# Kernel tuning notes

Measured on AMD Instinct MI355X. Metric: run time of the kernel, lower is better.

## Reference

```python
import jax, jax.numpy as jnp
import numpy as np

WS = 7          # window size
SHIFT = 3       # shift size
HEADS = 4
DIM = 128
PRETRAIN = 7    # pretrain_window_size
LN_EPS = 1e-3   # keras LayerNormalization default epsilon

# ---- constant relative-position structures (match TF meshgrid 'xy' indexing) ----
def _rel_index(ws):
    coords = np.stack(np.meshgrid(np.arange(ws), np.arange(ws)))  # [2, ws, ws] (xy)
    flat = coords.reshape(2, -1)
    rel = (flat[:, :, None] - flat[:, None, :]).transpose(1, 2, 0)  # [N, N, 2]
    ry = (rel[..., 0] + ws - 1) * (2 * ws - 1)
    rx = rel[..., 1] + ws - 1
    return (ry + rx).reshape(-1)  # [N*N]

def _rel_table(ws, pretrain):
    h = np.arange(-(ws - 1), ws, dtype=np.float32)
    t = np.stack(np.meshgrid(h, h), axis=-1)[None]  # [1, 2ws-1, 2ws-1, 2] (xy)
    t = t / (pretrain - 1)
    t = t * (8.0 / (pretrain - 1))
    return np.sign(t) * np.log1p(np.abs(t)) / np.log(8.0)

REL_INDEX = jnp.asarray(_rel_index(WS))
REL_TABLE = jnp.asarray(_rel_table(WS, PRETRAIN))


def layernorm(x, g, b, eps=LN_EPS):
    m = jnp.mean(x, axis=-1, keepdims=True)
    v = jnp.mean(jnp.square(x - m), axis=-1, keepdims=True)
    return (x - m) / jnp.sqrt(v + eps) * g + b


def setup_inputs() -> dict:
    key = jax.random.key(0)
    ks = jax.random.split(key, 16)
    B, H, W, C = 64, 56, 56, DIM
    nW = (H // WS) * (W // WS)
    hid = int(C * 4.0)
    rpe_h = 512
    def w(k, shape, scale=0.02):
        return jax.random.normal(k, shape, dtype=jnp.float32) * scale
    return {
        "x": jax.random.normal(ks[0], (B, H, W, C), dtype=jnp.float32),
        "mask_matrix": jax.random.normal(ks[1], (nW, WS * WS, WS * WS), dtype=jnp.float32),
        "norm1_g": jnp.ones((C,), jnp.float32),
        "norm1_b": jnp.zeros((C,), jnp.float32),
        "qkv_w": w(ks[2], (C, 3 * C)),
        "q_bias": jnp.zeros((C,), jnp.float32),
        "v_bias": jnp.zeros((C,), jnp.float32),
        "logit_scale": jnp.full((HEADS, 1, 1), np.log(10.0), jnp.float32),
        "rpe_w1": w(ks[3], (2, rpe_h)),
        "rpe_b1": jnp.zeros((rpe_h,), jnp.float32),
        "rpe_w2": w(ks[4], (rpe_h, HEADS)),
        "proj_w": w(ks[5], (C, C)),
        "proj_b": jnp.zeros((C,), jnp.float32),
        "norm2_g": jnp.ones((C,), jnp.float32),
        "norm2_b": jnp.zeros((C,), jnp.float32),
        "fc1_w": w(ks[6], (C, hid)),
        "fc1_b": jnp.zeros((hid,), jnp.float32),
        "fc2_w": w(ks[7], (hid, C)),
        "fc2_b": jnp.zeros((C,), jnp.float32),
    }


def reference(x, mask_matrix, norm1_g, norm1_b, qkv_w, q_bias, v_bias, logit_scale,
              rpe_w1, rpe_b1, rpe_w2, proj_w, proj_b, norm2_g, norm2_b,
              fc1_w, fc1_b, fc2_w, fc2_b):
    B, H, W, C = x.shape
    N = WS * WS
    hd = C // HEADS
    shortcut = x

    # cyclic shift + window partition -> [Bw, N, C]
    xs = jnp.roll(x, (-SHIFT, -SHIFT), axis=(1, 2))
    xw = xs.reshape(B, H // WS, WS, W // WS, WS, C).transpose(0, 1, 3, 2, 4, 5)
    xw = xw.reshape(-1, N, C)
    Bw = xw.shape[0]

    # qkv with (q_bias, 0, v_bias)
    qkv_bias = jnp.concatenate([q_bias, jnp.zeros_like(v_bias), v_bias])
    qkv = (xw @ qkv_w + qkv_bias).reshape(Bw, N, 3, HEADS, hd).transpose(2, 0, 3, 1, 4)
    q, k, v = qkv[0], qkv[1], qkv[2]  # [Bw, HEADS, N, hd]

    # cosine attention with clamped learnable log-scale
    scale = jnp.exp(jnp.minimum(logit_scale, jnp.log(1.0 / 0.01)))
    qn = q / jnp.sqrt(jnp.maximum(jnp.sum(q * q, -1, keepdims=True), 1e-12))
    kn = k / jnp.sqrt(jnp.maximum(jnp.sum(k * k, -1, keepdims=True), 1e-12))
    attn = jnp.einsum('bhnd,bhmd->bhnm', qn, kn) * scale

    # continuous relative position bias via tiny MLP
    t = REL_TABLE.reshape(-1, 2)                          # [(2ws-1)^2, 2]
    bias_table = jax.nn.relu(t @ rpe_w1 + rpe_b1) @ rpe_w2  # [(2ws-1)^2, HEADS]
    pb = bias_table[REL_INDEX].reshape(N, N, HEADS).transpose(2, 0, 1)
    attn = attn + (16.0 * jax.nn.sigmoid(pb))[None]

    # shift mask
    nW = mask_matrix.shape[0]
    attn = attn.reshape(Bw // nW, nW, HEADS, N, N) + mask_matrix[None, :, None]
    attn = attn.reshape(-1, HEADS, N, N)

    attn = jax.nn.softmax(attn, axis=-1)
    out = jnp.einsum('bhnm,bhmd->bhnd', attn, v).transpose(0, 2, 1, 3).reshape(Bw, N, C)
    out = out @ proj_w + proj_b

    # window reverse + un-shift
    out = out.reshape(B, H // WS, W // WS, WS, WS, C).transpose(0, 1, 3, 2, 4, 5)
    out = out.reshape(B, H, W, C)
    out = jnp.roll(out, (SHIFT, SHIFT), axis=(1, 2))

    # post-norm residuals (SwinV2 style)
    x = shortcut + layernorm(out, norm1_g, norm1_b)
    h = jax.nn.gelu(x @ fc1_w + fc1_b, approximate=False) @ fc2_w + fc2_b
    x = x + layernorm(h, norm2_g, norm2_b)
    return x
```

## Files before the change

kernel.cpp:

```cpp
#include <hip/hip_runtime.h>

typedef __attribute__((ext_vector_type(8))) short bf16x8;
typedef __attribute__((ext_vector_type(4))) float f32x4;

__device__ __forceinline__ short f2bf(float f) {
    union { float f; unsigned u; } c; c.f = f;
    unsigned r = c.u + 0x7FFFu + ((c.u >> 16) & 1u);
    return (short)(r >> 16);
}
__device__ __forceinline__ float bf2f(short s) {
    union { unsigned u; float f; } c; c.u = ((unsigned)(unsigned short)s) << 16;
    return c.f;
}

#define MFMA(a, b, c) __builtin_amdgcn_mfma_f32_16x16x32_bf16((a), (b), (c), 0, 0, 0)

#define WS_QKVWT   0
#define WS_PROJWT  98304
#define WS_FC1WT   131072
#define WS_FC2WT   262144
#define WS_PB16    393216
#define WS_COMB    434176

__global__ __launch_bounds__(256) void k_prep_w(
    const float* __restrict__ qkv_w, const float* __restrict__ proj_w,
    const float* __restrict__ fc1_w, const float* __restrict__ fc2_w,
    short* __restrict__ qkv_wt, short* __restrict__ proj_wt,
    short* __restrict__ fc1_wt, short* __restrict__ fc2_wt) {
    int id = blockIdx.x * 256 + threadIdx.x;
    if (id < 49152) {
        int n = id >> 7, k = id & 127;
        qkv_wt[id] = f2bf(qkv_w[k * 384 + n]);
    } else if (id < 65536) {
        int i = id - 49152; int n = i >> 7, k = i & 127;
        proj_wt[i] = f2bf(proj_w[k * 128 + n]);
    } else if (id < 131072) {
        int i = id - 65536; int n = i >> 7, k = i & 127;
        fc1_wt[i] = f2bf(fc1_w[k * 512 + n]);
    } else if (id < 196608) {
        int i = id - 131072; int n = i >> 9, k = i & 511;
        fc2_wt[i] = f2bf(fc2_w[k * 128 + n]);
    }
}

__device__ __forceinline__ float rpe_f(float u) {
    float us = u * (2.0f / 9.0f);
    return copysignf(log1pf(fabsf(us)), us) * 0.48089834696298783f;
}

__global__ __launch_bounds__(256) void k_prep_bias(
    const float* __restrict__ w1, const float* __restrict__ b1,
    const float* __restrict__ w2, float* __restrict__ pb16) {
    __shared__ float bt[169][4];
    int tid = threadIdx.x;
    if (tid < 169) {
        int i = tid / 13, j = tid - 13 * (tid / 13);
        float t0 = rpe_f((float)(j - 6));
        float t1 = rpe_f((float)(i - 6));
        float a0 = 0.f, a1 = 0.f, a2 = 0.f, a3 = 0.f;
        for (int k = 0; k < 512; ++k) {
            float r = fmaxf(t0 * w1[k] + t1 * w1[512 + k] + b1[k], 0.f);
            a0 += r * w2[k * 4 + 0]; a1 += r * w2[k * 4 + 1];
            a2 += r * w2[k * 4 + 2]; a3 += r * w2[k * 4 + 3];
        }
        bt[tid][0] = a0; bt[tid][1] = a1; bt[tid][2] = a2; bt[tid][3] = a3;
    }
    __syncthreads();
    for (int idx = tid; idx < 9604; idx += 256) {
        int h = idx / 2401, pq = idx - 2401 * h;
        int p = pq / 49, q = pq - 49 * p;
        int dx = p % 7 - q % 7;
        int dy = p / 7 - q / 7;
        int m = (dx + 6) * 13 + (dy + 6);
        float v = bt[m][h];
        pb16[idx] = 16.0f / (1.0f + expf(-v));
    }
}

__global__ __launch_bounds__(256) void k_combine(
    const float* __restrict__ mask, const float* __restrict__ pb16,
    float* __restrict__ comb) {
    int idx = blockIdx.x * 256 + threadIdx.x;
    if (idx >= 614656) return;
    int w = idx / 9604, rem = idx - 9604 * w;
    int pq = rem % 2401;
    comb[idx] = mask[w * 2401 + pq] + pb16[rem];
}

__global__ __launch_bounds__(256) void k_attn(
    const float* __restrict__ x, const float* __restrict__ comb,
    const short* __restrict__ qkv_wt, const short* __restrict__ proj_wt,
    const float* __restrict__ q_bias, const float* __restrict__ v_bias,
    const float* __restrict__ logit_scale, const float* __restrict__ proj_b,
    const float* __restrict__ n1g, const float* __restrict__ n1b,
    float* __restrict__ out) {
    __shared__ short sm[29504];
    short* q_s = sm;
    short* k_s = sm + 7840;
    short* v_s = sm + 15680;
    short* p_s = sm + 24896;
    short* xw  = sm;

    const int tid = threadIdx.x;
    const int lane = tid & 63, wv = tid >> 6;
    const int n16 = lane & 15, q4 = lane >> 4;
    const int wb = blockIdx.x;
    const int bb = wb >> 6, widx = wb & 63;
    const int wy = widx >> 3, wx = widx & 7;

    if (tid < 196) {
        int tok = tid >> 2, part = tid & 3;
        int ty = tok / 7, tx = tok - 7 * ty;
        int sy = wy * 7 + ty + 3; if (sy >= 56) sy -= 56;
        int sx = wx * 7 + tx + 3; if (sx >= 56) sx -= 56;
        const float* src = x + (((bb * 56 + sy) * 56 + sx) << 7) + part * 32;
        short* dst = xw + tok * 136 + part * 32;
#pragma unroll
        for (int j = 0; j < 8; ++j) {
            float4 v = *(const float4*)(src + j * 4);
            short4 o;
            o.x = f2bf(v.x); o.y = f2bf(v.y); o.z = f2bf(v.z); o.w = f2bf(v.w);
            *(short4*)(dst + j * 4) = o;
        }
    }
    __syncthreads();

    bf16x8 afr[4][4];
#pragma unroll
    for (int mt = 0; mt < 4; ++mt)
#pragma unroll
        for (int ks = 0; ks < 4; ++ks)
            afr[mt][ks] = *(const bf16x8*)(xw + (mt * 16 + n16) * 136 + ks * 32 + q4 * 8);

    f32x4 acc[6][4];
#pragma unroll
    for (int ntl = 0; ntl < 6; ++ntl) {
        int n = (wv * 6 + ntl) * 16 + n16;
        bf16x8 bfr[4];
#pragma unroll
        for (int ks = 0; ks < 4; ++ks)
            bfr[ks] = *(const bf16x8*)(qkv_wt + n * 128 + ks * 32 + q4 * 8);
#pragma unroll
        for (int mt = 0; mt < 4; ++mt) {
            f32x4 a = {0.f, 0.f, 0.f, 0.f};
#pragma unroll
            for (int ks = 0; ks < 4; ++ks) a = MFMA(afr[mt][ks], bfr[ks], a);
            acc[ntl][mt] = a;
        }
    }
    __syncthreads();

#pragma unroll
    for (int ntl = 0; ntl < 6; ++ntl) {
        int n = (wv * 6 + ntl) * 16 + n16;
        int sec = n >> 7, h = (n >> 5) & 3, chn = n & 31;
        float bias = (sec == 0) ? q_bias[n] : ((sec == 2) ? v_bias[n & 127] : 0.f);
#pragma unroll
        for (int mt = 0; mt < 4; ++mt) {
#pragma unroll
            for (int reg = 0; reg < 4; ++reg) {
                int r = mt * 16 + q4 * 4 + reg;
                float val = acc[ntl][mt][reg] + bias;
                if (sec == 2) {
                    v_s[h * 2304 + chn * 72 + r] = (r < 49) ? f2bf(val) : (short)0;
                } else if (r < 49) {
                    short* base = sec ? k_s : q_s;
                    base[h * 1960 + r * 40 + chn] = f2bf(val);
                }
            }
        }
    }
    __syncthreads();

    for (int i = tid; i < 392; i += 256) {
        int which = (i >= 196) ? 1 : 0;
        int rem = i - which * 196;
        int h = rem / 49, t = rem - 49 * h;
        short* row = (which ? k_s : q_s) + h * 1960 + t * 40;
        float vv[32]; float ss = 0.f;
#pragma unroll
        for (int j = 0; j < 8; ++j) {
            short4 s4 = *(const short4*)(row + j * 4);
            vv[j*4+0] = bf2f(s4.x); vv[j*4+1] = bf2f(s4.y);
            vv[j*4+2] = bf2f(s4.z); vv[j*4+3] = bf2f(s4.w);
            ss += vv[j*4+0]*vv[j*4+0] + vv[j*4+1]*vv[j*4+1]
                + vv[j*4+2]*vv[j*4+2] + vv[j*4+3]*vv[j*4+3];
        }
        float inv = 1.0f / sqrtf(fmaxf(ss, 1e-12f));
        if (!which) inv *= expf(fminf(logit_scale[h], 4.6051702f));
#pragma unroll
        for (int j = 0; j < 8; ++j) {
            short4 o;
            o.x = f2bf(vv[j*4+0]*inv); o.y = f2bf(vv[j*4+1]*inv);
            o.z = f2bf(vv[j*4+2]*inv); o.w = f2bf(vv[j*4+3]*inv);
            *(short4*)(row + j * 4) = o;
        }
    }
    __syncthreads();

    const int rb = wv * 16;
#pragma unroll 1
    for (int h = 0; h < 4; ++h) {
        bf16x8 aq = *(const bf16x8*)(q_s + h * 1960 + (rb + n16) * 40 + q4 * 8);
        f32x4 s[4];
#pragma unroll
        for (int nt = 0; nt < 4; ++nt) {
            bf16x8 bk = *(const bf16x8*)(k_s + h * 1960 + (nt * 16 + n16) * 40 + q4 * 8);
            f32x4 z = {0.f, 0.f, 0.f, 0.f};
            s[nt] = MFMA(aq, bk, z);
        }
#pragma unroll
        for (int nt = 0; nt < 4; ++nt) {
            int c = nt * 16 + n16;
#pragma unroll
            for (int reg = 0; reg < 4; ++reg) {
                int r = rb + q4 * 4 + reg;
                float val;
                if (c < 49) {
                    val = s[nt][reg];
                    if (r < 49) val += comb[((widx * 4 + h) * 49 + r) * 49 + c];
                } else val = -INFINITY;
                s[nt][reg] = val;
            }
        }
#pragma unroll
        for (int reg = 0; reg < 4; ++reg) {
            float m = fmaxf(fmaxf(s[0][reg], s[1][reg]), fmaxf(s[2][reg], s[3][reg]));
#pragma unroll
            for (int d = 1; d < 16; d <<= 1) m = fmaxf(m, __shfl_xor(m, d, 64));
            float e0 = expf(s[0][reg] - m), e1 = expf(s[1][reg] - m);
            float e2 = expf(s[2][reg] - m), e3 = expf(s[3][reg] - m);
            float sum = e0 + e1 + e2 + e3;
#pragma unroll
            for (int d = 1; d < 16; d <<= 1) sum += __shfl_xor(sum, d, 64);
            float inv = 1.0f / sum;
            s[0][reg] = e0 * inv; s[1][reg] = e1 * inv;
            s[2][reg] = e2 * inv; s[3][reg] = e3 * inv;
        }
#pragma unroll
        for (int nt = 0; nt < 4; ++nt)
#pragma unroll
            for (int reg = 0; reg < 4; ++reg)
                p_s[wv * 1152 + (q4 * 4 + reg) * 72 + nt * 16 + n16] = f2bf(s[nt][reg]);

        bf16x8 ap0 = *(const bf16x8*)(p_s + wv * 1152 + n16 * 72 + q4 * 8);
        bf16x8 ap1 = *(const bf16x8*)(p_s + wv * 1152 + n16 * 72 + 32 + q4 * 8);
#pragma unroll
        for (int nt2 = 0; nt2 < 2; ++nt2) {
            bf16x8 bv0 = *(const bf16x8*)(v_s + h * 2304 + (nt2 * 16 + n16) * 72 + q4 * 8);
            bf16x8 bv1 = *(const bf16x8*)(v_s + h * 2304 + (nt2 * 16 + n16) * 72 + 32 + q4 * 8);
            f32x4 z = {0.f, 0.f, 0.f, 0.f};
            f32x4 o = MFMA(ap0, bv0, z);
            o = MFMA(ap1, bv1, o);
#pragma unroll
            for (int reg = 0; reg < 4; ++reg) {
                int r = rb + q4 * 4 + reg;
                if (r < 49)
                    q_s[h * 1960 + r * 40 + nt2 * 16 + n16] = f2bf(o[reg]);
            }
        }
    }

    bf16x8 apj[4];
#pragma unroll
    for (int ks = 0; ks < 4; ++ks)
        apj[ks] = *(const bf16x8*)(q_s + ks * 1960 + (rb + n16) * 40 + q4 * 8);
    f32x4 pacc[8];
#pragma unroll
    for (int nt = 0; nt < 8; ++nt) {
        f32x4 a = {0.f, 0.f, 0.f, 0.f};
#pragma unroll
        for (int ks = 0; ks < 4; ++ks) {
            bf16x8 bp = *(const bf16x8*)(proj_wt + (nt * 16 + n16) * 128 + ks * 32 + q4 * 8);
            a = MFMA(apj[ks], bp, a);
        }
        pacc[nt] = a;
    }

    float pbv[8], gv[8], bvv[8];
#pragma unroll
    for (int nt = 0; nt < 8; ++nt) {
        int c = nt * 16 + n16;
        pbv[nt] = proj_b[c]; gv[nt] = n1g[c]; bvv[nt] = n1b[c];
    }
#pragma unroll
    for (int reg = 0; reg < 4; ++reg) {
        int r = rb + q4 * 4 + reg;
        float vals[8]; float s1 = 0.f, s2 = 0.f;
#pragma unroll
        for (int nt = 0; nt < 8; ++nt) {
            float v = pacc[nt][reg] + pbv[nt];
            vals[nt] = v; s1 += v; s2 += v * v;
        }
#pragma unroll
        for (int d = 1; d < 16; d <<= 1) {
            s1 += __shfl_xor(s1, d, 64);
            s2 += __shfl_xor(s2, d, 64);
        }
        float mean = s1 * 0.0078125f;
        float var = s2 * 0.0078125f - mean * mean;
        float inv = 1.0f / sqrtf(var + 1e-3f);
        if (r < 49) {
            int ty = r / 7, tx = r - 7 * ty;
            int fy = wy * 7 + ty + 3; if (fy >= 56) fy -= 56;
            int fx = wx * 7 + tx + 3; if (fx >= 56) fx -= 56;
            int gb = ((bb * 56 + fy) * 56 + fx) << 7;
#pragma unroll
            for (int nt = 0; nt < 8; ++nt) {
                int c = nt * 16 + n16;
                float ln = (vals[nt] - mean) * inv * gv[nt] + bvv[nt];
                out[gb + c] = x[gb + c] + ln;
            }
        }
    }
}

__global__ __launch_bounds__(256) void k_mlp(
    float* __restrict__ io, const short* __restrict__ fc1_wt,
    const short* __restrict__ fc2_wt, const float* __restrict__ fc1_b,
    const float* __restrict__ fc2_b, const float* __restrict__ n2g,
    const float* __restrict__ n2b) {
    __shared__ short sm2[26624];
    short* xt = sm2;
    short* hc = sm2 + 17408;

    const int tid = threadIdx.x;
    const int lane = tid & 63, wv = tid >> 6;
    const int n16 = lane & 15, q4 = lane >> 4;
    const int T0 = blockIdx.x * 128;

    {
        int trow = tid >> 1, half = tid & 1;
        const float* src = io + (T0 + trow) * 128 + half * 64;
        short* dst = xt + trow * 136 + half * 64;
#pragma unroll
        for (int j = 0; j < 16; ++j) {
            float4 v = *(const float4*)(src + j * 4);
            short4 o;
            o.x = f2bf(v.x); o.y = f2bf(v.y); o.z = f2bf(v.z); o.w = f2bf(v.w);
            *(short4*)(dst + j * 4) = o;
        }
    }
    __syncthreads();

    f32x4 oacc[2][8];
#pragma unroll
    for (int i2 = 0; i2 < 2; ++i2)
#pragma unroll
        for (int nt = 0; nt < 8; ++nt) oacc[i2][nt] = (f32x4){0.f, 0.f, 0.f, 0.f};

#pragma unroll 1
    for (int ch = 0; ch < 8; ++ch) {
        int nrow = ch * 64 + wv * 16 + n16;
        bf16x8 b1[4];
#pragma unroll
        for (int ks = 0; ks < 4; ++ks)
            b1[ks] = *(const bf16x8*)(fc1_wt + nrow * 128 + ks * 32 + q4 * 8);
        float fb = fc1_b[nrow];
#pragma unroll
        for (int mt = 0; mt < 8; ++mt) {
            f32x4 a = {0.f, 0.f, 0.f, 0.f};
#pragma unroll
            for (int ks = 0; ks < 4; ++ks) {
                bf16x8 af = *(const bf16x8*)(xt + (mt * 16 + n16) * 136 + ks * 32 + q4 * 8);
                a = MFMA(af, b1[ks], a);
            }
#pragma unroll
            for (int reg = 0; reg < 4; ++reg) {
                float v = a[reg] + fb;
                float g = 0.5f * v * (1.0f + erff(v * 0.7071067811865476f));
                hc[(mt * 16 + q4 * 4 + reg) * 72 + wv * 16 + n16] = f2bf(g);
            }
        }
        __syncthreads();
        bf16x8 a2[2][2];
#pragma unroll
        for (int i2 = 0; i2 < 2; ++i2) {
            int m = (wv + i2 * 4) * 16;
#pragma unroll
            for (int ks2 = 0; ks2 < 2; ++ks2)
                a2[i2][ks2] = *(const bf16x8*)(hc + (m + n16) * 72 + ks2 * 32 + q4 * 8);
        }
#pragma unroll
        for (int nt2 = 0; nt2 < 8; ++nt2) {
#pragma unroll
            for (int ks2 = 0; ks2 < 2; ++ks2) {
                bf16x8 b2 = *(const bf16x8*)(fc2_wt + (nt2 * 16 + n16) * 512 + ch * 64 + ks2 * 32 + q4 * 8);
                oacc[0][nt2] = MFMA(a2[0][ks2], b2, oacc[0][nt2]);
                oacc[1][nt2] = MFMA(a2[1][ks2], b2, oacc[1][nt2]);
            }
        }
        __syncthreads();
    }

    float f2bv[8], g2[8], b2v[8];
#pragma unroll
    for (int nt2 = 0; nt2 < 8; ++nt2) {
        int c = nt2 * 16 + n16;
        f2bv[nt2] = fc2_b[c]; g2[nt2] = n2g[c]; b2v[nt2] = n2b[c];
    }
#pragma unroll
    for (int i2 = 0; i2 < 2; ++i2) {
        int rb2 = (wv + i2 * 4) * 16;
#pragma unroll
        for (int reg = 0; reg < 4; ++reg) {
            int r = rb2 + q4 * 4 + reg;
            float vals[8]; float s1 = 0.f, s2 = 0.f;
#pragma unroll
            for (int nt2 = 0; nt2 < 8; ++nt2) {
                float v = oacc[i2][nt2][reg] + f2bv[nt2];
                vals[nt2] = v; s1 += v; s2 += v * v;
            }
#pragma unroll
            for (int d = 1; d < 16; d <<= 1) {
                s1 += __shfl_xor(s1, d, 64);
                s2 += __shfl_xor(s2, d, 64);
            }
            float mean = s1 * 0.0078125f;
            float var = s2 * 0.0078125f - mean * mean;
            float inv = 1.0f / sqrtf(var + 1e-3f);
            int gb = (T0 + r) * 128;
#pragma unroll
            for (int nt2 = 0; nt2 < 8; ++nt2) {
                int c = nt2 * 16 + n16;
                float ln = (vals[nt2] - mean) * inv * g2[nt2] + b2v[nt2];
                io[gb + c] = io[gb + c] + ln;
            }
        }
    }
}

extern "C" void kernel_launch(void* const* d_in, const int* in_sizes, int n_in,
                              void* d_out, int out_size, void* d_ws, size_t ws_size,
                              hipStream_t stream) {
    const float* x      = (const float*)d_in[0];
    const float* mask   = (const float*)d_in[1];
    const float* n1g    = (const float*)d_in[2];
    const float* n1b    = (const float*)d_in[3];
    const float* qkv_w  = (const float*)d_in[4];
    const float* q_bias = (const float*)d_in[5];
    const float* v_bias = (const float*)d_in[6];
    const float* lscale = (const float*)d_in[7];
    const float* rpe_w1 = (const float*)d_in[8];
    const float* rpe_b1 = (const float*)d_in[9];
    const float* rpe_w2 = (const float*)d_in[10];
    const float* proj_w = (const float*)d_in[11];
    const float* proj_b = (const float*)d_in[12];
    const float* n2g    = (const float*)d_in[13];
    const float* n2b    = (const float*)d_in[14];
    const float* fc1_w  = (const float*)d_in[15];
    const float* fc1_b  = (const float*)d_in[16];
    const float* fc2_w  = (const float*)d_in[17];
    const float* fc2_b  = (const float*)d_in[18];

    char* ws = (char*)d_ws;
    short* qkv_wt  = (short*)(ws + WS_QKVWT);
    short* proj_wt = (short*)(ws + WS_PROJWT);
    short* fc1_wt  = (short*)(ws + WS_FC1WT);
    short* fc2_wt  = (short*)(ws + WS_FC2WT);
    float* pb16    = (float*)(ws + WS_PB16);
    float* comb    = (float*)(ws + WS_COMB);
    float* out     = (float*)d_out;

    k_prep_w<<<768, 256, 0, stream>>>(qkv_w, proj_w, fc1_w, fc2_w,
                                      qkv_wt, proj_wt, fc1_wt, fc2_wt);
    k_prep_bias<<<1, 256, 0, stream>>>(rpe_w1, rpe_b1, rpe_w2, pb16);
    k_combine<<<2401, 256, 0, stream>>>(mask, pb16, comb);
    k_attn<<<4096, 256, 0, stream>>>(x, comb, qkv_wt, proj_wt, q_bias, v_bias,
                                     lscale, proj_b, n1g, n1b, out);
    k_mlp<<<1568, 256, 0, stream>>>(out, fc1_wt, fc2_wt, fc1_b, fc2_b, n2g, n2b);
}
```

Baseline: 752.1 us.

## Rework attention and MLP kernels with swizzled LDS, max-free softmax, and tanh-GELU

Spreads the relative-position MLP over 169 blocks and folds a constant softmax shift into the bias table. The attention kernel uses XOR-swizzled shared-memory layouts to cut bank conflicts, prefetches the bias, drops the row-max reduction from softmax and defers normalisation until after the PV product. The MLP kernel gives each wave its own rows so the block-level barriers go away, and swaps erf GELU for a tanh/exp approximation. Occupancy hints, packed bf16 conversion and fast rsqrt/exp are added throughout, at the cost of softmax overflow risk and slightly different numerics.

```diff
diff --git a/kernel.cpp b/kernel.cpp
--- a/kernel.cpp
+++ b/kernel.cpp
@@ -1,4 +1,5 @@
 #include <hip/hip_runtime.h>
+#include <hip/hip_bf16.h>
 
 typedef __attribute__((ext_vector_type(8))) short bf16x8;
 typedef __attribute__((ext_vector_type(4))) float f32x4;
@@ -12,6 +13,11 @@
     union { unsigned u; float f; } c; c.u = ((unsigned)(unsigned short)s) << 16;
     return c.f;
 }
+__device__ __forceinline__ unsigned pk2(float a, float b) {
+    __hip_bfloat162 h2 = __float22bfloat162_rn(make_float2(a, b));
+    union { __hip_bfloat162 h; unsigned u; } c; c.h = h2;
+    return c.u;
+}
 
 #define MFMA(a, b, c) __builtin_amdgcn_mfma_f32_16x16x32_bf16((a), (b), (c), 0, 0, 0)
 
@@ -19,7 +25,7 @@
 #define WS_PROJWT  98304
 #define WS_FC1WT   131072
 #define WS_FC2WT   262144
-#define WS_PB16    393216
+#define WS_BT16    393216
 #define WS_COMB    434176
 
 __global__ __launch_bounds__(256) void k_prep_w(
@@ -48,58 +54,78 @@
     return copysignf(log1pf(fabsf(us)), us) * 0.48089834696298783f;
 }
 
-__global__ __launch_bounds__(256) void k_prep_bias(
+__global__ __launch_bounds__(256) void k_bias_table(
     const float* __restrict__ w1, const float* __restrict__ b1,
-    const float* __restrict__ w2, float* __restrict__ pb16) {
-    __shared__ float bt[169][4];
-    int tid = threadIdx.x;
-    if (tid < 169) {
-        int i = tid / 13, j = tid - 13 * (tid / 13);
-        float t0 = rpe_f((float)(j - 6));
-        float t1 = rpe_f((float)(i - 6));
-        float a0 = 0.f, a1 = 0.f, a2 = 0.f, a3 = 0.f;
-        for (int k = 0; k < 512; ++k) {
-            float r = fmaxf(t0 * w1[k] + t1 * w1[512 + k] + b1[k], 0.f);
-            a0 += r * w2[k * 4 + 0]; a1 += r * w2[k * 4 + 1];
-            a2 += r * w2[k * 4 + 2]; a3 += r * w2[k * 4 + 3];
-        }
-        bt[tid][0] = a0; bt[tid][1] = a1; bt[tid][2] = a2; bt[tid][3] = a3;
-    }
+    const float* __restrict__ w2, const float* __restrict__ ls,
+    float* __restrict__ bt16s) {
+    int m = blockIdx.x;
+    int i = m / 13, j = m - 13 * i;
+    float t0 = rpe_f((float)(j - 6));
+    float t1 = rpe_f((float)(i - 6));
+    float a0 = 0.f, a1 = 0.f, a2 = 0.f, a3 = 0.f;
+    for (int k = threadIdx.x; k < 512; k += 256) {
+        float r = fmaxf(t0 * w1[k] + t1 * w1[512 + k] + b1[k], 0.f);
+        a0 += r * w2[k * 4 + 0]; a1 += r * w2[k * 4 + 1];
+        a2 += r * w2[k * 4 + 2]; a3 += r * w2[k * 4 + 3];
+    }
+    __shared__ float red[4][4];
+#pragma unroll
+    for (int d = 1; d < 64; d <<= 1) {
+        a0 += __shfl_xor(a0, d, 64); a1 += __shfl_xor(a1, d, 64);
+        a2 += __shfl_xor(a2, d, 64); a3 += __shfl_xor(a3, d, 64);
+    }
+    int wv = threadIdx.x >> 6;
+    if ((threadIdx.x & 63) == 0) { red[wv][0] = a0; red[wv][1] = a1; red[wv][2] = a2; red[wv][3] = a3; }
     __syncthreads();
-    for (int idx = tid; idx < 9604; idx += 256) {
-        int h = idx / 2401, pq = idx - 2401 * h;
-        int p = pq / 49, q = pq - 49 * p;
-        int dx = p % 7 - q % 7;
-        int dy = p / 7 - q / 7;
-        int m = (dx + 6) * 13 + (dy + 6);
-        float v = bt[m][h];
-        pb16[idx] = 16.0f / (1.0f + expf(-v));
+    if (threadIdx.x < 4) {
+        int h = threadIdx.x;
+        float s = red[0][h] + red[1][h] + red[2][h] + red[3][h];
+        float sig = 16.f / (1.f + __expf(-s));
+        float sc = __expf(fminf(ls[h], 4.6051702f));
+        bt16s[m * 4 + h] = sig - sc - 8.f;
     }
 }
 
 __global__ __launch_bounds__(256) void k_combine(
-    const float* __restrict__ mask, const float* __restrict__ pb16,
+    const float* __restrict__ mask, const float* __restrict__ bt16s,
     float* __restrict__ comb) {
     int idx = blockIdx.x * 256 + threadIdx.x;
     if (idx >= 614656) return;
     int w = idx / 9604, rem = idx - 9604 * w;
-    int pq = rem % 2401;
-    comb[idx] = mask[w * 2401 + pq] + pb16[rem];
-}
-
-__global__ __launch_bounds__(256) void k_attn(
+    int h = rem / 2401, pq = rem - 2401 * h;
+    int p = pq / 49, q = pq - 49 * p;
+    int dx = p % 7 - q % 7;
+    int dy = p / 7 - q / 7;
+    int m = (dx + 6) * 13 + (dy + 6);
+    comb[idx] = mask[w * 2401 + pq] + bt16s[m * 4 + h];
+}
+
+#define QS_OFF 0
+#define KS_OFF 6272
+#define VS_OFF 14112
+#define PS_OFF 22304
+__device__ __forceinline__ int qs_addr(int h, int r, int c) {
+    return QS_OFF + h * 1568 + r * 32 + (c ^ (((r >> 1) & 3) << 3));
+}
+__device__ __forceinline__ int ks_addr(int h, int r, int c) {
+    return KS_OFF + h * 1960 + r * 40 + c;
+}
+__device__ __forceinline__ int vs_addr(int h, int c, int t) {
+    return VS_OFF + h * 2048 + c * 64 + (t ^ ((c & 7) << 3));
+}
+__device__ __forceinline__ int ps_addr(int w, int r, int c) {
+    return PS_OFF + w * 1024 + r * 64 + (c ^ ((r & 7) << 3));
+}
+
+__global__ __launch_bounds__(256, 3) void k_attn(
     const float* __restrict__ x, const float* __restrict__ comb,
     const short* __restrict__ qkv_wt, const short* __restrict__ proj_wt,
     const float* __restrict__ q_bias, const float* __restrict__ v_bias,
     const float* __restrict__ logit_scale, const float* __restrict__ proj_b,
     const float* __restrict__ n1g, const float* __restrict__ n1b,
     float* __restrict__ out) {
-    __shared__ short sm[29504];
-    short* q_s = sm;
-    short* k_s = sm + 7840;
-    short* v_s = sm + 15680;
-    short* p_s = sm + 24896;
-    short* xw  = sm;
+    __shared__ short sm[26400];
+    short* xw = sm;
 
     const int tid = threadIdx.x;
     const int lane = tid & 63, wv = tid >> 6;
@@ -116,11 +142,13 @@
         const float* src = x + (((bb * 56 + sy) * 56 + sx) << 7) + part * 32;
         short* dst = xw + tok * 136 + part * 32;
 #pragma unroll
-        for (int j = 0; j < 8; ++j) {
-            float4 v = *(const float4*)(src + j * 4);
-            short4 o;
-            o.x = f2bf(v.x); o.y = f2bf(v.y); o.z = f2bf(v.z); o.w = f2bf(v.w);
-            *(short4*)(dst + j * 4) = o;
+        for (int j = 0; j < 4; ++j) {
+            float4 a = *(const float4*)(src + j * 8);
+            float4 b = *(const float4*)(src + j * 8 + 4);
+            uint4 o;
+            o.x = pk2(a.x, a.y); o.y = pk2(a.z, a.w);
+            o.z = pk2(b.x, b.y); o.w = pk2(b.z, b.w);
+            *(uint4*)(dst + j * 8) = o;
         }
     }
     __syncthreads();
@@ -152,20 +180,34 @@
 
 #pragma unroll
     for (int ntl = 0; ntl < 6; ++ntl) {
-        int n = (wv * 6 + ntl) * 16 + n16;
-        int sec = n >> 7, h = (n >> 5) & 3, chn = n & 31;
-        float bias = (sec == 0) ? q_bias[n] : ((sec == 2) ? v_bias[n & 127] : 0.f);
-#pragma unroll
-        for (int mt = 0; mt < 4; ++mt) {
-#pragma unroll
-            for (int reg = 0; reg < 4; ++reg) {
-                int r = mt * 16 + q4 * 4 + reg;
-                float val = acc[ntl][mt][reg] + bias;
-                if (sec == 2) {
-                    v_s[h * 2304 + chn * 72 + r] = (r < 49) ? f2bf(val) : (short)0;
-                } else if (r < 49) {
-                    short* base = sec ? k_s : q_s;
-                    base[h * 1960 + r * 40 + chn] = f2bf(val);
+        int g = wv * 6 + ntl, sec = g >> 3;
+        if (sec == 2) {
+            int hv = (g >> 1) & 3;
+            int c32 = ((g & 1) << 4) + n16;
+            float bias = v_bias[(g - 16) * 16 + n16];
+#pragma unroll
+            for (int mt = 0; mt < 4; ++mt) {
+                int t0 = mt * 16 + q4 * 4;
+                short4 o;
+                o.x = (t0 + 0 < 49) ? f2bf(acc[ntl][mt][0] + bias) : (short)0;
+                o.y = (t0 + 1 < 49) ? f2bf(acc[ntl][mt][1] + bias) : (short)0;
+                o.z = (t0 + 2 < 49) ? f2bf(acc[ntl][mt][2] + bias) : (short)0;
+                o.w = (t0 + 3 < 49) ? f2bf(acc[ntl][mt][3] + bias) : (short)0;
+                *(short4*)(sm + vs_addr(hv, c32, t0)) = o;
+            }
+        } else {
+            int h = (g >> 1) & 3;
+            int chn = ((g & 1) << 4) + n16;
+            float bias = (sec == 0) ? q_bias[g * 16 + n16] : 0.f;
+#pragma unroll
+            for (int mt = 0; mt < 4; ++mt) {
+#pragma unroll
+                for (int reg = 0; reg < 4; ++reg) {
+                    int r = mt * 16 + q4 * 4 + reg;
+                    if (r < 49) {
+                        short vb = f2bf(acc[ntl][mt][reg] + bias);
+                        sm[sec == 0 ? qs_addr(h, r, chn) : ks_addr(h, r, chn)] = vb;
+                    }
                 }
             }
         }
@@ -174,26 +216,29 @@
 
     for (int i = tid; i < 392; i += 256) {
         int which = (i >= 196) ? 1 : 0;
-        int rem = i - which * 196;
+        int rem = i - 196 * which;
         int h = rem / 49, t = rem - 49 * h;
-        short* row = (which ? k_s : q_s) + h * 1960 + t * 40;
         float vv[32]; float ss = 0.f;
 #pragma unroll
-        for (int j = 0; j < 8; ++j) {
-            short4 s4 = *(const short4*)(row + j * 4);
-            vv[j*4+0] = bf2f(s4.x); vv[j*4+1] = bf2f(s4.y);
-            vv[j*4+2] = bf2f(s4.z); vv[j*4+3] = bf2f(s4.w);
-            ss += vv[j*4+0]*vv[j*4+0] + vv[j*4+1]*vv[j*4+1]
-                + vv[j*4+2]*vv[j*4+2] + vv[j*4+3]*vv[j*4+3];
-        }
-        float inv = 1.0f / sqrtf(fmaxf(ss, 1e-12f));
-        if (!which) inv *= expf(fminf(logit_scale[h], 4.6051702f));
-#pragma unroll
-        for (int j = 0; j < 8; ++j) {
-            short4 o;
-            o.x = f2bf(vv[j*4+0]*inv); o.y = f2bf(vv[j*4+1]*inv);
-            o.z = f2bf(vv[j*4+2]*inv); o.w = f2bf(vv[j*4+3]*inv);
-            *(short4*)(row + j * 4) = o;
+        for (int j = 0; j < 4; ++j) {
+            bf16x8 s8 = which ? *(const bf16x8*)(sm + ks_addr(h, t, j * 8))
+                              : *(const bf16x8*)(sm + qs_addr(h, t, j * 8));
+#pragma unroll
+            for (int e = 0; e < 8; ++e) {
+                float f = bf2f(s8[e]); vv[j * 8 + e] = f; ss += f * f;
+            }
+        }
+        float inv = __frsqrt_rn(fmaxf(ss, 1e-12f));
+        if (!which) inv *= __expf(fminf(logit_scale[h], 4.6051702f));
+#pragma unroll
+        for (int j = 0; j < 4; ++j) {
+            uint4 o;
+            o.x = pk2(vv[j*8+0] * inv, vv[j*8+1] * inv);
+            o.y = pk2(vv[j*8+2] * inv, vv[j*8+3] * inv);
+            o.z = pk2(vv[j*8+4] * inv, vv[j*8+5] * inv);
+            o.w = pk2(vv[j*8+6] * inv, vv[j*8+7] * inv);
+            if (which) *(uint4*)(sm + ks_addr(h, t, j * 8)) = o;
+            else       *(uint4*)(sm + qs_addr(h, t, j * 8)) = o;
         }
     }
     __syncthreads();
@@ -201,11 +246,22 @@
     const int rb = wv * 16;
 #pragma unroll 1
     for (int h = 0; h < 4; ++h) {
-        bf16x8 aq = *(const bf16x8*)(q_s + h * 1960 + (rb + n16) * 40 + q4 * 8);
+        const float* cb = comb + (widx * 4 + h) * 2401;
+        float cbv[4][4];
+#pragma unroll
+        for (int nt = 0; nt < 4; ++nt) {
+            int c = nt * 16 + n16;
+#pragma unroll
+            for (int reg = 0; reg < 4; ++reg) {
+                int r = rb + q4 * 4 + reg;
+                cbv[nt][reg] = (r < 49 && c < 49) ? cb[r * 49 + c] : 0.f;
+            }
+        }
+        bf16x8 aq = *(const bf16x8*)(sm + qs_addr(h, rb + n16, q4 * 8));
         f32x4 s[4];
 #pragma unroll
         for (int nt = 0; nt < 4; ++nt) {
-            bf16x8 bk = *(const bf16x8*)(k_s + h * 1960 + (nt * 16 + n16) * 40 + q4 * 8);
+            bf16x8 bk = *(const bf16x8*)(sm + ks_addr(h, nt * 16 + n16, q4 * 8));
             f32x4 z = {0.f, 0.f, 0.f, 0.f};
             s[nt] = MFMA(aq, bk, z);
         }
@@ -215,40 +271,29 @@
 #pragma unroll
             for (int reg = 0; reg < 4; ++reg) {
                 int r = rb + q4 * 4 + reg;
-                float val;
-                if (c < 49) {
-                    val = s[nt][reg];
-                    if (r < 49) val += comb[((widx * 4 + h) * 49 + r) * 49 + c];
-                } else val = -INFINITY;
-                s[nt][reg] = val;
-            }
-        }
+                s[nt][reg] = (r < 49 && c < 49) ? __expf(s[nt][reg] + cbv[nt][reg]) : 0.f;
+            }
+        }
+        float invr[4];
 #pragma unroll
         for (int reg = 0; reg < 4; ++reg) {
-            float m = fmaxf(fmaxf(s[0][reg], s[1][reg]), fmaxf(s[2][reg], s[3][reg]));
-#pragma unroll
-            for (int d = 1; d < 16; d <<= 1) m = fmaxf(m, __shfl_xor(m, d, 64));
-            float e0 = expf(s[0][reg] - m), e1 = expf(s[1][reg] - m);
-            float e2 = expf(s[2][reg] - m), e3 = expf(s[3][reg] - m);
-            float sum = e0 + e1 + e2 + e3;
-#pragma unroll
-            for (int d = 1; d < 16; d <<= 1) sum += __shfl_xor(sum, d, 64);
-            float inv = 1.0f / sum;
-            s[0][reg] = e0 * inv; s[1][reg] = e1 * inv;
-            s[2][reg] = e2 * inv; s[3][reg] = e3 * inv;
+            float t = s[0][reg] + s[1][reg] + s[2][reg] + s[3][reg];
+            t += __shfl_xor(t, 1, 64); t += __shfl_xor(t, 2, 64);
+            t += __shfl_xor(t, 4, 64); t += __shfl_xor(t, 8, 64);
+            invr[reg] = __builtin_amdgcn_rcpf(t);
         }
 #pragma unroll
         for (int nt = 0; nt < 4; ++nt)
 #pragma unroll
             for (int reg = 0; reg < 4; ++reg)
-                p_s[wv * 1152 + (q4 * 4 + reg) * 72 + nt * 16 + n16] = f2bf(s[nt][reg]);
-
-        bf16x8 ap0 = *(const bf16x8*)(p_s + wv * 1152 + n16 * 72 + q4 * 8);
-        bf16x8 ap1 = *(const bf16x8*)(p_s + wv * 1152 + n16 * 72 + 32 + q4 * 8);
+                sm[ps_addr(wv, q4 * 4 + reg, nt * 16 + n16)] = f2bf(s[nt][reg]);
+
+        bf16x8 ap0 = *(const bf16x8*)(sm + ps_addr(wv, n16, q4 * 8));
+        bf16x8 ap1 = *(const bf16x8*)(sm + ps_addr(wv, n16, 32 + q4 * 8));
 #pragma unroll
         for (int nt2 = 0; nt2 < 2; ++nt2) {
-            bf16x8 bv0 = *(const bf16x8*)(v_s + h * 2304 + (nt2 * 16 + n16) * 72 + q4 * 8);
-            bf16x8 bv1 = *(const bf16x8*)(v_s + h * 2304 + (nt2 * 16 + n16) * 72 + 32 + q4 * 8);
+            bf16x8 bv0 = *(const bf16x8*)(sm + vs_addr(h, nt2 * 16 + n16, q4 * 8));
+            bf16x8 bv1 = *(const bf16x8*)(sm + vs_addr(h, nt2 * 16 + n16, 32 + q4 * 8));
             f32x4 z = {0.f, 0.f, 0.f, 0.f};
             f32x4 o = MFMA(ap0, bv0, z);
             o = MFMA(ap1, bv1, o);
@@ -256,7 +301,7 @@
             for (int reg = 0; reg < 4; ++reg) {
                 int r = rb + q4 * 4 + reg;
                 if (r < 49)
-                    q_s[h * 1960 + r * 40 + nt2 * 16 + n16] = f2bf(o[reg]);
+                    sm[qs_addr(h, r, nt2 * 16 + n16)] = f2bf(o[reg] * invr[reg]);
             }
         }
     }
@@ -264,7 +309,7 @@
     bf16x8 apj[4];
 #pragma unroll
     for (int ks = 0; ks < 4; ++ks)
-        apj[ks] = *(const bf16x8*)(q_s + ks * 1960 + (rb + n16) * 40 + q4 * 8);
+        apj[ks] = *(const bf16x8*)(sm + qs_addr(ks, rb + n16, q4 * 8));
     f32x4 pacc[8];
 #pragma unroll
     for (int nt = 0; nt < 8; ++nt) {
@@ -299,7 +344,7 @@
         }
         float mean = s1 * 0.0078125f;
         float var = s2 * 0.0078125f - mean * mean;
-        float inv = 1.0f / sqrtf(var + 1e-3f);
+        float inv = __frsqrt_rn(var + 1e-3f);
         if (r < 49) {
             int ty = r / 7, tx = r - 7 * ty;
             int fy = wy * 7 + ty + 3; if (fy >= 56) fy -= 56;
@@ -315,100 +360,106 @@
     }
 }
 
-__global__ __launch_bounds__(256) void k_mlp(
+__global__ __launch_bounds__(256, 3) void k_mlp(
     float* __restrict__ io, const short* __restrict__ fc1_wt,
     const short* __restrict__ fc2_wt, const float* __restrict__ fc1_b,
     const float* __restrict__ fc2_b, const float* __restrict__ n2g,
     const float* __restrict__ n2b) {
     __shared__ short sm2[26624];
-    short* xt = sm2;
-    short* hc = sm2 + 17408;
-
     const int tid = threadIdx.x;
     const int lane = tid & 63, wv = tid >> 6;
     const int n16 = lane & 15, q4 = lane >> 4;
     const int T0 = blockIdx.x * 128;
+    const int rowbase = wv * 32;
+    short* xt = sm2;
+    short* hcw = sm2 + 17408 + wv * 2304;
 
     {
-        int trow = tid >> 1, half = tid & 1;
-        const float* src = io + (T0 + trow) * 128 + half * 64;
-        short* dst = xt + trow * 136 + half * 64;
-#pragma unroll
-        for (int j = 0; j < 16; ++j) {
-            float4 v = *(const float4*)(src + j * 4);
-            short4 o;
-            o.x = f2bf(v.x); o.y = f2bf(v.y); o.z = f2bf(v.z); o.w = f2bf(v.w);
-            *(short4*)(dst + j * 4) = o;
-        }
-    }
-    __syncthreads();
+        int r = rowbase + (lane >> 1), half = lane & 1;
+        const float* src = io + (T0 + r) * 128 + half * 64;
+        short* dst = xt + r * 136 + half * 64;
+#pragma unroll
+        for (int j = 0; j < 8; ++j) {
+            float4 a = *(const float4*)(src + j * 8);
+            float4 b = *(const float4*)(src + j * 8 + 4);
+            uint4 o;
+            o.x = pk2(a.x, a.y); o.y = pk2(a.z, a.w);
+            o.z = pk2(b.x, b.y); o.w = pk2(b.z, b.w);
+            *(uint4*)(dst + j * 8) = o;
+        }
+    }
+
+    bf16x8 af[2][4];
+#pragma unroll
+    for (int mt = 0; mt < 2; ++mt)
+#pragma unroll
+        for (int ks = 0; ks < 4; ++ks)
+            af[mt][ks] = *(const bf16x8*)(xt + (rowbase + mt * 16 + n16) * 136 + ks * 32 + q4 * 8);
 
     f32x4 oacc[2][8];
 #pragma unroll
-    for (int i2 = 0; i2 < 2; ++i2)
-#pragma unroll
-        for (int nt = 0; nt < 8; ++nt) oacc[i2][nt] = (f32x4){0.f, 0.f, 0.f, 0.f};
+    for (int mt = 0; mt < 2; ++mt)
+#pragma unroll
+        for (int nt = 0; nt < 8; ++nt) oacc[mt][nt] = (f32x4){0.f, 0.f, 0.f, 0.f};
 
 #pragma unroll 1
     for (int ch = 0; ch < 8; ++ch) {
-        int nrow = ch * 64 + wv * 16 + n16;
-        bf16x8 b1[4];
-#pragma unroll
-        for (int ks = 0; ks < 4; ++ks)
-            b1[ks] = *(const bf16x8*)(fc1_wt + nrow * 128 + ks * 32 + q4 * 8);
-        float fb = fc1_b[nrow];
-#pragma unroll
-        for (int mt = 0; mt < 8; ++mt) {
-            f32x4 a = {0.f, 0.f, 0.f, 0.f};
-#pragma unroll
-            for (int ks = 0; ks < 4; ++ks) {
-                bf16x8 af = *(const bf16x8*)(xt + (mt * 16 + n16) * 136 + ks * 32 + q4 * 8);
-                a = MFMA(af, b1[ks], a);
-            }
-#pragma unroll
-            for (int reg = 0; reg < 4; ++reg) {
-                float v = a[reg] + fb;
-                float g = 0.5f * v * (1.0f + erff(v * 0.7071067811865476f));
-                hc[(mt * 16 + q4 * 4 + reg) * 72 + wv * 16 + n16] = f2bf(g);
-            }
-        }
-        __syncthreads();
+#pragma unroll
+        for (int nt = 0; nt < 4; ++nt) {
+            int nrow = ch * 64 + nt * 16 + n16;
+            bf16x8 b1v[4];
+#pragma unroll
+            for (int ks = 0; ks < 4; ++ks)
+                b1v[ks] = *(const bf16x8*)(fc1_wt + nrow * 128 + ks * 32 + q4 * 8);
+            float fb = fc1_b[nrow];
+#pragma unroll
+            for (int mt = 0; mt < 2; ++mt) {
+                f32x4 a = {0.f, 0.f, 0.f, 0.f};
+#pragma unroll
+                for (int ks = 0; ks < 4; ++ks) a = MFMA(af[mt][ks], b1v[ks], a);
+#pragma unroll
+                for (int reg = 0; reg < 4; ++reg) {
+                    float v = a[reg] + fb;
+                    float u2 = v * (1.5957691216f + 0.0713548162f * v * v);
+                    u2 = fminf(fmaxf(u2, -40.f), 40.f);
+                    float ex = __expf(u2);
+                    float g = v * ex * __builtin_amdgcn_rcpf(ex + 1.f);
+                    hcw[(mt * 16 + q4 * 4 + reg) * 72 + nt * 16 + n16] = f2bf(g);
+                }
+            }
+        }
         bf16x8 a2[2][2];
 #pragma unroll
-        for (int i2 = 0; i2 < 2; ++i2) {
-            int m = (wv + i2 * 4) * 16;
-#pragma unroll
-            for (int ks2 = 0; ks2 < 2; ++ks2)
-                a2[i2][ks2] = *(const bf16x8*)(hc + (m + n16) * 72 + ks2 * 32 + q4 * 8);
-        }
+        for (int mt = 0; mt < 2; ++mt)
+#pragma unroll
+            for (int kc = 0; kc < 2; ++kc)
+                a2[mt][kc] = *(const bf16x8*)(hcw + (mt * 16 + n16) * 72 + kc * 32 + q4 * 8);
 #pragma unroll
         for (int nt2 = 0; nt2 < 8; ++nt2) {
 #pragma unroll
-            for (int ks2 = 0; ks2 < 2; ++ks2) {
-                bf16x8 b2 = *(const bf16x8*)(fc2_wt + (nt2 * 16 + n16) * 512 + ch * 64 + ks2 * 32 + q4 * 8);
-                oacc[0][nt2] = MFMA(a2[0][ks2], b2, oacc[0][nt2]);
-                oacc[1][nt2] = MFMA(a2[1][ks2], b2, oacc[1][nt2]);
-            }
-        }
-        __syncthreads();
-    }
-
-    float f2bv[8], g2[8], b2v[8];
+            for (int kc = 0; kc < 2; ++kc) {
+                bf16x8 b2 = *(const bf16x8*)(fc2_wt + (nt2 * 16 + n16) * 512 + ch * 64 + kc * 32 + q4 * 8);
+                oacc[0][nt2] = MFMA(a2[0][kc], b2, oacc[0][nt2]);
+                oacc[1][nt2] = MFMA(a2[1][kc], b2, oacc[1][nt2]);
+            }
+        }
+    }
+
+    float f2v[8], g2[8], b2v[8];
 #pragma unroll
     for (int nt2 = 0; nt2 < 8; ++nt2) {
         int c = nt2 * 16 + n16;
-        f2bv[nt2] = fc2_b[c]; g2[nt2] = n2g[c]; b2v[nt2] = n2b[c];
-    }
-#pragma unroll
-    for (int i2 = 0; i2 < 2; ++i2) {
-        int rb2 = (wv + i2 * 4) * 16;
+        f2v[nt2] = fc2_b[c]; g2[nt2] = n2g[c]; b2v[nt2] = n2b[c];
+    }
+#pragma unroll
+    for (int mt = 0; mt < 2; ++mt) {
 #pragma unroll
         for (int reg = 0; reg < 4; ++reg) {
-            int r = rb2 + q4 * 4 + reg;
+            int tl = mt * 16 + q4 * 4 + reg;
             float vals[8]; float s1 = 0.f, s2 = 0.f;
 #pragma unroll
             for (int nt2 = 0; nt2 < 8; ++nt2) {
-                float v = oacc[i2][nt2][reg] + f2bv[nt2];
+                float v = oacc[mt][nt2][reg] + f2v[nt2];
                 vals[nt2] = v; s1 += v; s2 += v * v;
             }
 #pragma unroll
@@ -418,8 +469,8 @@
             }
             float mean = s1 * 0.0078125f;
             float var = s2 * 0.0078125f - mean * mean;
-            float inv = 1.0f / sqrtf(var + 1e-3f);
-            int gb = (T0 + r) * 128;
+            float inv = __frsqrt_rn(var + 1e-3f);
+            int gb = (T0 + rowbase + tl) * 128;
 #pragma unroll
             for (int nt2 = 0; nt2 < 8; ++nt2) {
                 int c = nt2 * 16 + n16;
@@ -458,14 +509,14 @@
     short* proj_wt = (short*)(ws + WS_PROJWT);
     short* fc1_wt  = (short*)(ws + WS_FC1WT);
     short* fc2_wt  = (short*)(ws + WS_FC2WT);
-    float* pb16    = (float*)(ws + WS_PB16);
+    float* bt16s   = (float*)(ws + WS_BT16);
     float* comb    = (float*)(ws + WS_COMB);
     float* out     = (float*)d_out;
 
     k_prep_w<<<768, 256, 0, stream>>>(qkv_w, proj_w, fc1_w, fc2_w,
                                       qkv_wt, proj_wt, fc1_wt, fc2_wt);
-    k_prep_bias<<<1, 256, 0, stream>>>(rpe_w1, rpe_b1, rpe_w2, pb16);
-    k_combine<<<2401, 256, 0, stream>>>(mask, pb16, comb);
+    k_bias_table<<<169, 256, 0, stream>>>(rpe_w1, rpe_b1, rpe_w2, lscale, bt16s);
+    k_combine<<<2401, 256, 0, stream>>>(mask, bt16s, comb);
     k_attn<<<4096, 256, 0, stream>>>(x, comb, qkv_wt, proj_wt, q_bias, v_bias,
                                      lscale, proj_b, n1g, n1b, out);
     k_mlp<<<1568, 256, 0, stream>>>(out, fc1_wt, fc2_wt, fc1_b, fc2_b, n2g, n2b);
```

Result: faster. 612.9 us (-18.5%).
